# Performance work log

Measured on AMD Instinct MI355X. Metric: run time of the kernel, lower is better.

## Reference

```python
import jax, jax.numpy as jnp
import numpy as np

N_NODES = 25000
N_EDGES = 400000
N_GRAPHS = 64
F_IN = 128


def setup_inputs() -> dict:
    key = jax.random.key(0)
    ks = jax.random.split(key, 16)
    inp = {}
    inp["x"] = jax.random.normal(ks[0], (N_NODES, F_IN), dtype=jnp.float32)
    inp["edge_index"] = jax.random.randint(ks[1], (2, N_EDGES), 0, N_NODES, dtype=jnp.int64)
    inp["edge_attr"] = jax.random.uniform(ks[2], (N_EDGES,), dtype=jnp.float32)
    inp["batch_ids"] = jnp.sort(jax.random.randint(ks[3], (N_NODES,), 0, N_GRAPHS, dtype=jnp.int64))
    def lin(k, fan_in, fan_out):
        bound = 1.0 / np.sqrt(fan_in)
        return jax.random.uniform(k, (fan_in, fan_out), dtype=jnp.float32, minval=-bound, maxval=bound)
    inp["W1_rel"] = lin(ks[4], F_IN, 512)
    inp["b1"] = jnp.zeros((512,), jnp.float32)
    inp["W1_root"] = lin(ks[5], F_IN, 512)
    inp["W2_rel"] = lin(ks[6], 512, 512)
    inp["b2"] = jnp.zeros((512,), jnp.float32)
    inp["W2_root"] = lin(ks[7], 512, 512)
    inp["Wl1"] = lin(ks[8], 512, 64)
    inp["bl1"] = jnp.zeros((64,), jnp.float32)
    inp["Wl2"] = lin(ks[9], 64, 16)
    inp["bl2"] = jnp.zeros((16,), jnp.float32)
    inp["Wl3"] = lin(ks[10], 16, 1)
    inp["bl3"] = jnp.zeros((1,), jnp.float32)
    return inp


def _graph_conv(h, src, dst, edge_attr, W_rel, b_rel, W_root, n_nodes):
    # PyG GraphConv: lin_rel(scatter_add(w_e * x_src, dst)) + lin_root(x)
    msg = h[src] * edge_attr[:, None]                       # [E, F] gather
    agg = jax.ops.segment_sum(msg, dst, num_segments=n_nodes)  # [N, F] scatter-add
    return agg @ W_rel + b_rel + h @ W_root


def reference(x, edge_index, edge_attr, batch_ids, W1_rel, b1, W1_root,
              W2_rel, b2, W2_root, Wl1, bl1, Wl2, bl2, Wl3, bl3):
    n_nodes = x.shape[0]
    src, dst = edge_index[0], edge_index[1]
    h = jax.nn.relu(_graph_conv(x, src, dst, edge_attr, W1_rel, b1, W1_root, n_nodes))
    h = jax.nn.relu(_graph_conv(h, src, dst, edge_attr, W2_rel, b2, W2_root, n_nodes))
    # global mean pool by graph id
    sums = jax.ops.segment_sum(h, batch_ids, num_segments=N_GRAPHS)  # [G, 512]
    counts = jax.ops.segment_sum(jnp.ones((n_nodes,), h.dtype), batch_ids, num_segments=N_GRAPHS)
    g = sums / jnp.maximum(counts, 1.0)[:, None]
    # dropout is identity in eval mode
    g = jax.nn.relu(g @ Wl1 + bl1)
    g = jax.nn.relu(g @ Wl2 + bl2)
    return g @ Wl3 + bl3  # [G, 1]
```

## Files before the change

### kernel.cpp

```cpp
#include <hip/hip_runtime.h>
#include <hip/hip_bf16.h>
#include <hip/hip_fp16.h>
#include <stdint.h>

#define N_NODESC 25000
#define N_EDGESC 400000
#define N_GRAPHSC 64
#define F_INC 128
#define HIDC 512
#define PSTRIDE 1600000

typedef __attribute__((ext_vector_type(8))) short short8;
typedef __attribute__((ext_vector_type(8))) _Float16 half8;
typedef __attribute__((ext_vector_type(4))) float f32x4;

__device__ __forceinline__ unsigned short f2h(float f) {
  return __half_as_ushort(__float2half_rn(f));
}

__global__ __launch_bounds__(256)
void prep_kernel(const float* __restrict__ x, const int* __restrict__ ei,
                 const float* __restrict__ W1rel, const float* __restrict__ W1root,
                 const float* __restrict__ W2rel, const float* __restrict__ W2root,
                 unsigned short* __restrict__ xp, unsigned short* __restrict__ W1T,
                 unsigned short* __restrict__ W2T, int* __restrict__ deg,
                 float* __restrict__ gsum) {
  int blk = blockIdx.x, t = threadIdx.x;
  if (blk < 1563) {
    int e = blk * 256 + t;
    if (e < N_EDGESC) atomicAdd(&deg[ei[N_EDGESC + e]], 1);
  } else if (blk < 4688) {
    int idx = ((blk - 1563) * 256 + t) * 4;
    int node = idx >> 7;
    int col = idx & 127;
    float4 v = *(const float4*)(x + idx);
    ushort4 o;
    o.x = f2h(v.x); o.y = f2h(v.y); o.z = f2h(v.z); o.w = f2h(v.w);
    *(ushort4*)(xp + (size_t)(col >> 6) * PSTRIDE + (size_t)node * 64 + (col & 63)) = o;
  } else if (blk < 4848) {
    __shared__ float tile[64][65];
    int b2 = blk - 4688;
    const float* src;
    unsigned short* dst;
    int n0, k0, Kout;
    if (b2 < 128) {
      int kt = b2 >> 3, nt = b2 & 7;
      k0 = kt * 64; n0 = nt * 64;
      src = (k0 < 512) ? (W2rel + (size_t)k0 * 512) : (W2root + (size_t)(k0 - 512) * 512);
      dst = W2T; Kout = 1024;
    } else {
      int b = b2 - 128;
      int kt = b >> 3, nt = b & 7;
      k0 = kt * 64; n0 = nt * 64;
      src = (k0 < 128) ? (W1rel + (size_t)k0 * 512) : (W1root + (size_t)(k0 - 128) * 512);
      dst = W1T; Kout = 256;
    }
    int c = t & 63;
    int r4 = t >> 6;
#pragma unroll
    for (int rr = 0; rr < 64; rr += 4) {
      int row = rr + r4;
      tile[c][row] = src[(size_t)row * 512 + n0 + c];
    }
    __syncthreads();
#pragma unroll
    for (int rr = 0; rr < 64; rr += 4) {
      int nrow = rr + r4;
      dst[(size_t)(n0 + nrow) * Kout + k0 + c] = f2h(tile[nrow][c]);
    }
  } else {
    int i = (blk - 4848) * 256 + t;
    if (i < N_GRAPHSC * HIDC) gsum[i] = 0.f;
  }
}

__global__ __launch_bounds__(1024)
void scan_kernel(const int* __restrict__ deg, int* __restrict__ indptr, int* __restrict__ cursor,
                 int* __restrict__ sorted) {
  __shared__ int binsS[1024];
  __shared__ int scan2[1024];
  __shared__ int Wsh[16];
  __shared__ int waveBase[16];
  __shared__ int gTot;
  const int t = threadIdx.x;
  const int w = t >> 6;
  const int lane = t & 63;
  const int stripe = t & 3;
  const int nbase = w * 1600;
  const unsigned ub = (unsigned)deg[N_NODESC];
  binsS[t] = 0;
  __syncthreads();

  int dl[25];
  int tw = 0;
#pragma unroll
  for (int i = 0; i < 25; ++i) {
    int idx = nbase + i * 64 + lane;
    int d = (idx < N_NODESC) ? (int)((unsigned)deg[idx] - ub) : 0;
    dl[i] = d;
    if (idx < N_NODESC) {
      tw += d;
      atomicAdd(&binsS[(d > 255 ? 255 : d) * 4 + stripe], 1);
    }
  }
#pragma unroll
  for (int off = 32; off > 0; off >>= 1) tw += __shfl_xor(tw, off);
  if (lane == 0) Wsh[w] = tw;
  __syncthreads();

  if (t < 16) {
    int v = Wsh[t];
    int s = v;
#pragma unroll
    for (int off = 1; off < 16; off <<= 1) {
      int u = __shfl_up(s, off);
      if (t >= off) s += u;
    }
    waveBase[t] = s - v;
    if (t == 15) gTot = s;
  }
  int bv = binsS[t];
  scan2[t] = bv;
  __syncthreads();
  for (int off = 1; off < 1024; off <<= 1) {
    int v2 = (t >= off) ? scan2[t - off] : 0;
    __syncthreads();
    scan2[t] += v2;
    __syncthreads();
  }
  binsS[t] = scan2[t] - bv;
  __syncthreads();

  int run = waveBase[w];
#pragma unroll
  for (int i = 0; i < 25; ++i) {
    int idx = nbase + i * 64 + lane;
    int d = dl[i];
    int s = d;
#pragma unroll
    for (int off = 1; off < 64; off <<= 1) {
      int u = __shfl_up(s, off);
      if (lane >= off) s += u;
    }
    int excl = run + s - d;
    if (idx < N_NODESC) {
      indptr[idx] = excl;
      cursor[idx] = excl;
      int fb = (d > 255 ? 255 : d) * 4 + stripe;
      int pos = atomicAdd(&binsS[fb], 1);
      sorted[pos] = idx;
    }
    run += __shfl(s, 63);
  }
  if (t == 0) indptr[N_NODESC] = gTot;
}

__global__ void fill_kernel(const int* __restrict__ ei, const float* __restrict__ ea,
                            int* __restrict__ cursor, unsigned* __restrict__ emeta) {
  int e = blockIdx.x * blockDim.x + threadIdx.x;
  if (e >= N_EDGESC) return;
  int dst = ei[N_EDGESC + e];
  int pos = atomicAdd(&cursor[dst], 1);
  unsigned short hw = __half_as_ushort(__float2half_rn(ea[e]));
  emeta[pos] = (unsigned)ei[e] | ((unsigned)hw << 16);
}

__global__ __launch_bounds__(256)
void agg_gather_s(const unsigned short* __restrict__ feat, const int* __restrict__ indptr,
                  const unsigned* __restrict__ emeta, const int* __restrict__ sorted,
                  unsigned short* __restrict__ outp, int lgP) {
  int panel = blockIdx.x & ((1 << lgP) - 1);
  int nidx = (blockIdx.x >> lgP) * 32 + (threadIdx.x >> 3);
  if (nidx >= N_NODESC) return;
  int c8 = threadIdx.x & 7;
  int node = sorted[nidx];
  int beg = indptr[node];
  int deg = indptr[node + 1] - beg;
  const unsigned* mp = emeta + beg;
  const char* fb = (const char*)(feat + (size_t)panel * PSTRIDE);
  unsigned coff = c8 * 16u;
  float acc0[8] = {}, acc1[8] = {};
  int j = 0;
  for (; j + 4 <= deg; j += 4) {
    unsigned m0_ = mp[j];
    unsigned m1_ = mp[j + 1];
    unsigned m2_ = mp[j + 2];
    unsigned m3_ = mp[j + 3];
    half8 v0 = *(const half8*)(fb + (m0_ & 0xffffu) * 128u + coff);
    half8 v1 = *(const half8*)(fb + (m1_ & 0xffffu) * 128u + coff);
    half8 v2 = *(const half8*)(fb + (m2_ & 0xffffu) * 128u + coff);
    half8 v3 = *(const half8*)(fb + (m3_ & 0xffffu) * 128u + coff);
    float w0 = __half2float(__ushort_as_half((unsigned short)(m0_ >> 16)));
    float w1 = __half2float(__ushort_as_half((unsigned short)(m1_ >> 16)));
    float w2 = __half2float(__ushort_as_half((unsigned short)(m2_ >> 16)));
    float w3 = __half2float(__ushort_as_half((unsigned short)(m3_ >> 16)));
#pragma unroll
    for (int c = 0; c < 8; ++c) acc0[c] += (float)v0[c] * w0;
#pragma unroll
    for (int c = 0; c < 8; ++c) acc1[c] += (float)v1[c] * w1;
#pragma unroll
    for (int c = 0; c < 8; ++c) acc0[c] += (float)v2[c] * w2;
#pragma unroll
    for (int c = 0; c < 8; ++c) acc1[c] += (float)v3[c] * w3;
  }
  if (j + 2 <= deg) {
    unsigned mA = mp[j];
    unsigned mB = mp[j + 1];
    half8 vA = *(const half8*)(fb + (mA & 0xffffu) * 128u + coff);
    half8 vB = *(const half8*)(fb + (mB & 0xffffu) * 128u + coff);
    float wA = __half2float(__ushort_as_half((unsigned short)(mA >> 16)));
    float wB = __half2float(__ushort_as_half((unsigned short)(mB >> 16)));
#pragma unroll
    for (int c = 0; c < 8; ++c) acc0[c] += (float)vA[c] * wA;
#pragma unroll
    for (int c = 0; c < 8; ++c) acc1[c] += (float)vB[c] * wB;
    j += 2;
  }
  if (j < deg) {
    unsigned mA = mp[j];
    half8 vA = *(const half8*)(fb + (mA & 0xffffu) * 128u + coff);
    float wA = __half2float(__ushort_as_half((unsigned short)(mA >> 16)));
#pragma unroll
    for (int c = 0; c < 8; ++c) acc0[c] += (float)vA[c] * wA;
  }
  half8 o;
#pragma unroll
  for (int c = 0; c < 8; ++c) o[c] = (_Float16)(acc0[c] + acc1[c]);
  *(half8*)(outp + (size_t)panel * PSTRIDE + (size_t)node * 64 + c8 * 8) = o;
}

__device__ __forceinline__ void gemm_map3(int b, int& m0, int& n0) {
  int g = (b & 7) * 98 + (b >> 3);
  m0 = (g >> 2) << 7;
  n0 = (g & 3) << 7;
}

__device__ __forceinline__ void stage_a(const short* Apan, int m0, int M,
                                        short* dst, int wave, int lane) {
#pragma unroll
  for (int i = 0; i < 4; ++i) {
    int s = ((i * 4 + wave) << 6) + lane;
    int row = s >> 3;
    int c = (s & 7) ^ (row & 7);
    int rg = m0 + row;
    if (rg > M - 1) rg = M - 1;
    const short* gp = Apan + (size_t)rg * 64 + (c << 3);
    __builtin_amdgcn_global_load_lds(
        (const __attribute__((address_space(1))) void*)gp,
        (__attribute__((address_space(3))) void*)(dst + ((i * 4 + wave) << 9)),
        16, 0, 0);
  }
}

__device__ __forceinline__ void stage_b(const short* BT, int n0, int K, int kbase,
                                        short* dst, int wave, int lane) {
#pragma unroll
  for (int i = 0; i < 4; ++i) {
    int s = ((i * 4 + wave) << 6) + lane;
    int row = s >> 3;
    int c = (s & 7) ^ (row & 7);
    const short* gp = BT + (size_t)(n0 + row) * K + kbase + (c << 3);
    __builtin_amdgcn_global_load_lds(
        (const __attribute__((address_space(1))) void*)gp,
        (__attribute__((address_space(3))) void*)(dst + ((i * 4 + wave) << 9)),
        16, 0, 0);
  }
}

__device__ __forceinline__ const short* apan_sel(const short* A0, const short* A1,
                                                 int S, int kt) {
  int kb = kt << 6;
  const short* Ab = (kb < S) ? A0 : A1;
  int koff = (kb < S) ? kb : kb - S;
  return Ab + (size_t)(koff >> 6) * PSTRIDE;
}

__device__ __forceinline__ void wg_barrier() {
  asm volatile("" ::: "memory");
  __builtin_amdgcn_s_barrier();
  asm volatile("" ::: "memory");
}

__device__ __forceinline__ void gemm_core(const short* A0, const short* A1,
                                          const short* BT, int M, int S,
                                          int m0, int n0, short* As, short* Bs,
                                          f32x4 (&acc)[4][4]) {
  const int K = 2 * S;
  const int nk = K >> 6;
  const int tid = threadIdx.x;
  const int wave = tid >> 6;
  const int lane = tid & 63;
  const int quad = lane >> 4;
  const int r = lane & 15;
  const int wm = (wave >> 1) << 6;
  const int wn = (wave & 1) << 6;

  int aoff[2][4], boff[2][4];
#pragma unroll
  for (int p = 0; p < 2; ++p) {
#pragma unroll
    for (int tm = 0; tm < 4; ++tm) {
      int ml = wm + tm * 16 + r;
      int c = (p << 2) + quad;
      aoff[p][tm] = (ml * 8 + (c ^ (ml & 7))) * 8;
    }
#pragma unroll
    for (int tn = 0; tn < 4; ++tn) {
      int nl = wn + tn * 16 + r;
      int c = (p << 2) + quad;
      boff[p][tn] = (nl * 8 + (c ^ (nl & 7))) * 8;
    }
  }

  stage_a(apan_sel(A0, A1, S, 0), m0, M, As, wave, lane);
  stage_b(BT, n0, K, 0, Bs, wave, lane);
  asm volatile("s_waitcnt vmcnt(0)");
  wg_barrier();

  for (int t = 0; t < nk; ++t) {
    const int cur = t & 1;
    const int nxt = cur ^ 1;
    int kt1 = (t + 1 < nk) ? t + 1 : nk - 1;
    stage_a(apan_sel(A0, A1, S, kt1), m0, M, As + nxt * 8192, wave, lane);
    stage_b(BT, n0, K, kt1 << 6, Bs + nxt * 8192, wave, lane);

    const short* Ac = As + cur * 8192;
    const short* Bc = Bs + cur * 8192;
    {
      half8 af[4], bf[4];
#pragma unroll
      for (int tm = 0; tm < 4; ++tm) af[tm] = *(const half8*)&Ac[aoff[0][tm]];
#pragma unroll
      for (int tn = 0; tn < 4; ++tn) bf[tn] = *(const half8*)&Bc[boff[0][tn]];
      __builtin_amdgcn_s_setprio(1);
#pragma unroll
      for (int tm = 0; tm < 4; ++tm)
#pragma unroll
        for (int tn = 0; tn < 4; ++tn)
          acc[tm][tn] = __builtin_amdgcn_mfma_f32_16x16x32_f16(af[tm], bf[tn], acc[tm][tn], 0, 0, 0);
      __builtin_amdgcn_s_setprio(0);
    }
    {
      half8 af[4], bf[4];
#pragma unroll
      for (int tm = 0; tm < 4; ++tm) af[tm] = *(const half8*)&Ac[aoff[1][tm]];
#pragma unroll
      for (int tn = 0; tn < 4; ++tn) bf[tn] = *(const half8*)&Bc[boff[1][tn]];
      __builtin_amdgcn_s_setprio(1);
#pragma unroll
      for (int tm = 0; tm < 4; ++tm)
#pragma unroll
        for (int tn = 0; tn < 4; ++tn)
          acc[tm][tn] = __builtin_amdgcn_mfma_f32_16x16x32_f16(af[tm], bf[tn], acc[tm][tn], 0, 0, 0);
      __builtin_amdgcn_s_setprio(0);
    }
    asm volatile("s_waitcnt vmcnt(0)");
    wg_barrier();
  }
}

__global__ __launch_bounds__(256, 2)
void gemm_bt_relu(const short* __restrict__ A0, const short* __restrict__ A1,
                  const short* __restrict__ BT, const float* __restrict__ bias,
                  unsigned short* __restrict__ Outp, int M, int S) {
  __shared__ __align__(16) short As[2 * 8192];
  __shared__ __align__(16) short Bs[2 * 8192];
  int m0, n0;
  gemm_map3(blockIdx.x, m0, n0);
  const int wave = threadIdx.x >> 6;
  const int lane = threadIdx.x & 63;
  const int quad = lane >> 4;
  const int r = lane & 15;
  const int wm = (wave >> 1) << 6;
  const int wn = (wave & 1) << 6;

  f32x4 acc[4][4] = {};
  gemm_core(A0, A1, BT, M, S, m0, n0, As, Bs, acc);

#pragma unroll
  for (int tm = 0; tm < 4; ++tm) {
    int rowb = m0 + wm + tm * 16 + quad * 4;
#pragma unroll
    for (int tn = 0; tn < 4; ++tn) {
      int col = n0 + wn + tn * 16 + r;
      float bv = bias[col];
      unsigned short* obase = Outp + (size_t)(col >> 6) * PSTRIDE + (col & 63);
#pragma unroll
      for (int reg = 0; reg < 4; ++reg) {
        int rr = rowb + reg;
        if (rr < M) {
          float v = acc[tm][tn][reg] + bv;
          v = v > 0.f ? v : 0.f;
          obase[(size_t)rr * 64] = f2h(v);
        }
      }
    }
  }
}

__global__ __launch_bounds__(256, 2)
void gemm_bt_pool(const short* __restrict__ A0, const short* __restrict__ A1,
                  const short* __restrict__ BT, const float* __restrict__ bias,
                  const int* __restrict__ batch, float* __restrict__ gsum, int M, int S) {
  __shared__ __align__(16) short As[2 * 8192];
  __shared__ __align__(16) short Bs[2 * 8192];
  int m0, n0;
  gemm_map3(blockIdx.x, m0, n0);
  const int wave = threadIdx.x >> 6;
  const int lane = threadIdx.x & 63;
  const int quad = lane >> 4;
  const int r = lane & 15;
  const int wm = (wave >> 1) << 6;
  const int wn = (wave & 1) << 6;

  f32x4 acc[4][4] = {};
  gemm_core(A0, A1, BT, M, S, m0, n0, As, Bs, acc);

  int gid[4][4];
#pragma unroll
  for (int tm = 0; tm < 4; ++tm) {
    int rowb = m0 + wm + tm * 16 + quad * 4;
#pragma unroll
    for (int reg = 0; reg < 4; ++reg) {
      int rr = rowb + reg;
      gid[tm][reg] = batch[rr < M ? rr : (M - 1)];
    }
#pragma unroll
    for (int tn = 0; tn < 4; ++tn) {
      float bv = bias[n0 + wn + tn * 16 + r];
#pragma unroll
      for (int reg = 0; reg < 4; ++reg) {
        int rr = rowb + reg;
        float v = acc[tm][tn][reg] + bv;
        v = v > 0.f ? v : 0.f;
        acc[tm][tn][reg] = (rr < M) ? v : 0.f;
      }
    }
  }
  int g_lo = batch[m0 < M ? m0 : (M - 1)];
  int g_hi = batch[(m0 + 127) < M ? (m0 + 127) : (M - 1)];
  for (int g = g_lo; g <= g_hi; ++g) {
#pragma unroll
    for (int tn = 0; tn < 4; ++tn) {
      float s = 0.f;
#pragma unroll
      for (int tm = 0; tm < 4; ++tm)
#pragma unroll
        for (int reg = 0; reg < 4; ++reg)
          s += (gid[tm][reg] == g) ? acc[tm][tn][reg] : 0.f;
      s += __shfl_xor(s, 16);
      s += __shfl_xor(s, 32);
      if (quad == 0)
        atomicAdd(&gsum[(size_t)g * HIDC + n0 + wn + tn * 16 + r], s);
    }
  }
}

__global__ __launch_bounds__(256)
void mlp_kernel(const float* __restrict__ gsum, const int* __restrict__ batch,
                const float* __restrict__ Wl1, const float* __restrict__ bl1,
                const float* __restrict__ Wl2, const float* __restrict__ bl2,
                const float* __restrict__ Wl3, const float* __restrict__ bl3,
                float* __restrict__ out) {
  int gi = blockIdx.x;
  int t = threadIdx.x;
  int unit = t & 63;
  int part = t >> 6;
  __shared__ float red[4][64];
  __shared__ float h1s[64];
  __shared__ float h2s[16];
  int lo = 0, hi = N_NODESC;
  while (lo < hi) { int mid = (lo + hi) >> 1; if (batch[mid] < gi) lo = mid + 1; else hi = mid; }
  int start = lo;
  hi = N_NODESC;
  while (lo < hi) { int mid = (lo + hi) >> 1; if (batch[mid] < gi + 1) lo = mid + 1; else hi = mid; }
  float inv = 1.0f / fmaxf((float)(lo - start), 1.0f);
  const float* gr = gsum + gi * HIDC;
  float acc = 0.f;
  for (int j = part * 128; j < (part + 1) * 128; ++j)
    acc += gr[j] * Wl1[j * 64 + unit];
  red[part][unit] = acc;
  __syncthreads();
  if (t < 64) {
    float a = bl1[t] + (red[0][t] + red[1][t] + red[2][t] + red[3][t]) * inv;
    h1s[t] = fmaxf(a, 0.f);
  }
  __syncthreads();
  if (t < 16) {
    float a = bl2[t];
    for (int j = 0; j < 64; ++j) a += h1s[j] * Wl2[j * 16 + t];
    h2s[t] = fmaxf(a, 0.f);
  }
  __syncthreads();
  if (t == 0) {
    float a = bl3[0];
    for (int j = 0; j < 16; ++j) a += h2s[j] * Wl3[j];
    out[gi] = a;
  }
}

extern "C" void kernel_launch(void* const* d_in, const int* in_sizes, int n_in,
                              void* d_out, int out_size, void* d_ws, size_t ws_size,
                              hipStream_t stream) {
  const float* x      = (const float*)d_in[0];
  const int*   ei     = (const int*)d_in[1];
  const float* ea     = (const float*)d_in[2];
  const int*   batch  = (const int*)d_in[3];
  const float* W1rel  = (const float*)d_in[4];
  const float* b1     = (const float*)d_in[5];
  const float* W1root = (const float*)d_in[6];
  const float* W2rel  = (const float*)d_in[7];
  const float* b2     = (const float*)d_in[8];
  const float* W2root = (const float*)d_in[9];
  const float* Wl1    = (const float*)d_in[10];
  const float* bl1    = (const float*)d_in[11];
  const float* Wl2    = (const float*)d_in[12];
  const float* bl2    = (const float*)d_in[13];
  const float* Wl3    = (const float*)d_in[14];
  const float* bl3    = (const float*)d_in[15];
  float* out = (float*)d_out;

  char* ws = (char*)d_ws;
  unsigned short* xp     = (unsigned short*)(ws + 0);
  unsigned short* agg1p  = (unsigned short*)(ws + 6400000);
  unsigned short* h1p    = (unsigned short*)(ws + 12800000);
  unsigned short* agg2p  = (unsigned short*)(ws + 38400000);
  unsigned short* W1T    = (unsigned short*)(ws + 64000000);
  unsigned short* W2T    = (unsigned short*)(ws + 64262144);
  float*          gsum   = (float*)(ws + 65310720);
  int*            deg    = (int*)(ws + 65441792);
  int*            cursor = (int*)(ws + 65541796);
  int*            indptr = (int*)(ws + 65641796);
  unsigned*       emeta  = (unsigned*)(ws + 65741812);
  int*            sorted = (int*)(ws + 67341812);

  prep_kernel<<<4976, 256, 0, stream>>>(x, ei, W1rel, W1root, W2rel, W2root,
                                        xp, W1T, W2T, deg, gsum);
  scan_kernel<<<1, 1024, 0, stream>>>(deg, indptr, cursor, sorted);
  fill_kernel<<<(N_EDGESC + 255) / 256, 256, 0, stream>>>(ei, ea, cursor, emeta);

  const int NBLK = (N_NODESC + 31) / 32;
  agg_gather_s<<<NBLK * 2, 256, 0, stream>>>(xp, indptr, emeta, sorted, agg1p, 1);

  gemm_bt_relu<<<784, 256, 0, stream>>>((const short*)agg1p, (const short*)xp,
                                        (const short*)W1T, b1, h1p, N_NODESC, 128);

  agg_gather_s<<<NBLK * 8, 256, 0, stream>>>(h1p, indptr, emeta, sorted, agg2p, 3);

  gemm_bt_pool<<<784, 256, 0, stream>>>((const short*)agg2p, (const short*)h1p,
                                        (const short*)W2T, b2, batch, gsum, N_NODESC, 512);

  mlp_kernel<<<N_GRAPHSC, 256, 0, stream>>>(gsum, batch, Wl1, bl1, Wl2, bl2, Wl3, bl3, out);
}
```

Baseline: 285.3 us.

## Enlarge GEMM tile to 256x128 and drop LDS double buffering

Both GEMM kernels move from 128x128 to 256x128 tiles, with each wave computing 128x64 using 8x4 MFMA accumulators, and the grid halves from 784 to 392 blocks. The double-buffered prefetch is replaced by a single-buffer loop: load, wait, barrier, compute, barrier. The aim is more reuse of each B tile and fewer blocks, at the cost of exposed global-load latency each k-step. Register pressure also rises, which may spill under launch_bounds(256,2), and 392 blocks may underfill the 256 CUs.

```diff
diff --git a/kernel.cpp b/kernel.cpp
--- a/kernel.cpp
+++ b/kernel.cpp
@@ -229,16 +229,16 @@
   *(half8*)(outp + (size_t)panel * PSTRIDE + (size_t)node * 64 + c8 * 8) = o;
 }
 
-__device__ __forceinline__ void gemm_map3(int b, int& m0, int& n0) {
-  int g = (b & 7) * 98 + (b >> 3);
-  m0 = (g >> 2) << 7;
+__device__ __forceinline__ void gemm_map4(int b, int& m0, int& n0) {
+  int g = (b & 7) * 49 + (b >> 3);
+  m0 = (g >> 2) << 8;
   n0 = (g & 3) << 7;
 }
 
-__device__ __forceinline__ void stage_a(const short* Apan, int m0, int M,
-                                        short* dst, int wave, int lane) {
-#pragma unroll
-  for (int i = 0; i < 4; ++i) {
+__device__ __forceinline__ void stage_a8(const short* Apan, int m0, int M,
+                                         short* dst, int wave, int lane) {
+#pragma unroll
+  for (int i = 0; i < 8; ++i) {
     int s = ((i * 4 + wave) << 6) + lane;
     int row = s >> 3;
     int c = (s & 7) ^ (row & 7);
@@ -252,8 +252,8 @@
   }
 }
 
-__device__ __forceinline__ void stage_b(const short* BT, int n0, int K, int kbase,
-                                        short* dst, int wave, int lane) {
+__device__ __forceinline__ void stage_b4(const short* BT, int n0, int K, int kbase,
+                                         short* dst, int wave, int lane) {
 #pragma unroll
   for (int i = 0; i < 4; ++i) {
     int s = ((i * 4 + wave) << 6) + lane;
@@ -284,7 +284,7 @@
 __device__ __forceinline__ void gemm_core(const short* A0, const short* A1,
                                           const short* BT, int M, int S,
                                           int m0, int n0, short* As, short* Bs,
-                                          f32x4 (&acc)[4][4]) {
+                                          f32x4 (&acc)[8][4]) {
   const int K = 2 * S;
   const int nk = K >> 6;
   const int tid = threadIdx.x;
@@ -292,14 +292,14 @@
   const int lane = tid & 63;
   const int quad = lane >> 4;
   const int r = lane & 15;
-  const int wm = (wave >> 1) << 6;
+  const int wm = (wave >> 1) << 7;
   const int wn = (wave & 1) << 6;
 
-  int aoff[2][4], boff[2][4];
+  int aoff[2][8], boff[2][4];
 #pragma unroll
   for (int p = 0; p < 2; ++p) {
 #pragma unroll
-    for (int tm = 0; tm < 4; ++tm) {
+    for (int tm = 0; tm < 8; ++tm) {
       int ml = wm + tm * 16 + r;
       int c = (p << 2) + quad;
       aoff[p][tm] = (ml * 8 + (c ^ (ml & 7))) * 8;
@@ -312,49 +312,39 @@
     }
   }
 
-  stage_a(apan_sel(A0, A1, S, 0), m0, M, As, wave, lane);
-  stage_b(BT, n0, K, 0, Bs, wave, lane);
-  asm volatile("s_waitcnt vmcnt(0)");
-  wg_barrier();
-
   for (int t = 0; t < nk; ++t) {
-    const int cur = t & 1;
-    const int nxt = cur ^ 1;
-    int kt1 = (t + 1 < nk) ? t + 1 : nk - 1;
-    stage_a(apan_sel(A0, A1, S, kt1), m0, M, As + nxt * 8192, wave, lane);
-    stage_b(BT, n0, K, kt1 << 6, Bs + nxt * 8192, wave, lane);
-
-    const short* Ac = As + cur * 8192;
-    const short* Bc = Bs + cur * 8192;
+    stage_a8(apan_sel(A0, A1, S, t), m0, M, As, wave, lane);
+    stage_b4(BT, n0, K, t << 6, Bs, wave, lane);
+    asm volatile("s_waitcnt vmcnt(0)");
+    wg_barrier();
     {
-      half8 af[4], bf[4];
-#pragma unroll
-      for (int tm = 0; tm < 4; ++tm) af[tm] = *(const half8*)&Ac[aoff[0][tm]];
-#pragma unroll
-      for (int tn = 0; tn < 4; ++tn) bf[tn] = *(const half8*)&Bc[boff[0][tn]];
+      half8 af[8], bf[4];
+#pragma unroll
+      for (int tm = 0; tm < 8; ++tm) af[tm] = *(const half8*)&As[aoff[0][tm]];
+#pragma unroll
+      for (int tn = 0; tn < 4; ++tn) bf[tn] = *(const half8*)&Bs[boff[0][tn]];
       __builtin_amdgcn_s_setprio(1);
 #pragma unroll
-      for (int tm = 0; tm < 4; ++tm)
+      for (int tm = 0; tm < 8; ++tm)
 #pragma unroll
         for (int tn = 0; tn < 4; ++tn)
           acc[tm][tn] = __builtin_amdgcn_mfma_f32_16x16x32_f16(af[tm], bf[tn], acc[tm][tn], 0, 0, 0);
       __builtin_amdgcn_s_setprio(0);
     }
     {
-      half8 af[4], bf[4];
-#pragma unroll
-      for (int tm = 0; tm < 4; ++tm) af[tm] = *(const half8*)&Ac[aoff[1][tm]];
-#pragma unroll
-      for (int tn = 0; tn < 4; ++tn) bf[tn] = *(const half8*)&Bc[boff[1][tn]];
+      half8 af[8], bf[4];
+#pragma unroll
+      for (int tm = 0; tm < 8; ++tm) af[tm] = *(const half8*)&As[aoff[1][tm]];
+#pragma unroll
+      for (int tn = 0; tn < 4; ++tn) bf[tn] = *(const half8*)&Bs[boff[1][tn]];
       __builtin_amdgcn_s_setprio(1);
 #pragma unroll
-      for (int tm = 0; tm < 4; ++tm)
+      for (int tm = 0; tm < 8; ++tm)
 #pragma unroll
         for (int tn = 0; tn < 4; ++tn)
           acc[tm][tn] = __builtin_amdgcn_mfma_f32_16x16x32_f16(af[tm], bf[tn], acc[tm][tn], 0, 0, 0);
       __builtin_amdgcn_s_setprio(0);
     }
-    asm volatile("s_waitcnt vmcnt(0)");
     wg_barrier();
   }
 }
@@ -363,22 +353,22 @@
 void gemm_bt_relu(const short* __restrict__ A0, const short* __restrict__ A1,
                   const short* __restrict__ BT, const float* __restrict__ bias,
                   unsigned short* __restrict__ Outp, int M, int S) {
-  __shared__ __align__(16) short As[2 * 8192];
-  __shared__ __align__(16) short Bs[2 * 8192];
+  __shared__ __align__(16) short As[256 * 64];
+  __shared__ __align__(16) short Bs[128 * 64];
   int m0, n0;
-  gemm_map3(blockIdx.x, m0, n0);
+  gemm_map4(blockIdx.x, m0, n0);
   const int wave = threadIdx.x >> 6;
   const int lane = threadIdx.x & 63;
   const int quad = lane >> 4;
   const int r = lane & 15;
-  const int wm = (wave >> 1) << 6;
+  const int wm = (wave >> 1) << 7;
   const int wn = (wave & 1) << 6;
 
-  f32x4 acc[4][4] = {};
+  f32x4 acc[8][4] = {};
   gemm_core(A0, A1, BT, M, S, m0, n0, As, Bs, acc);
 
 #pragma unroll
-  for (int tm = 0; tm < 4; ++tm) {
+  for (int tm = 0; tm < 8; ++tm) {
     int rowb = m0 + wm + tm * 16 + quad * 4;
 #pragma unroll
     for (int tn = 0; tn < 4; ++tn) {
@@ -402,23 +392,23 @@
 void gemm_bt_pool(const short* __restrict__ A0, const short* __restrict__ A1,
                   const short* __restrict__ BT, const float* __restrict__ bias,
                   const int* __restrict__ batch, float* __restrict__ gsum, int M, int S) {
-  __shared__ __align__(16) short As[2 * 8192];
-  __shared__ __align__(16) short Bs[2 * 8192];
+  __shared__ __align__(16) short As[256 * 64];
+  __shared__ __align__(16) short Bs[128 * 64];
   int m0, n0;
-  gemm_map3(blockIdx.x, m0, n0);
+  gemm_map4(blockIdx.x, m0, n0);
   const int wave = threadIdx.x >> 6;
   const int lane = threadIdx.x & 63;
   const int quad = lane >> 4;
   const int r = lane & 15;
-  const int wm = (wave >> 1) << 6;
+  const int wm = (wave >> 1) << 7;
   const int wn = (wave & 1) << 6;
 
-  f32x4 acc[4][4] = {};
+  f32x4 acc[8][4] = {};
   gemm_core(A0, A1, BT, M, S, m0, n0, As, Bs, acc);
 
-  int gid[4][4];
-#pragma unroll
-  for (int tm = 0; tm < 4; ++tm) {
+  int gid[8][4];
+#pragma unroll
+  for (int tm = 0; tm < 8; ++tm) {
     int rowb = m0 + wm + tm * 16 + quad * 4;
 #pragma unroll
     for (int reg = 0; reg < 4; ++reg) {
@@ -438,13 +428,13 @@
     }
   }
   int g_lo = batch[m0 < M ? m0 : (M - 1)];
-  int g_hi = batch[(m0 + 127) < M ? (m0 + 127) : (M - 1)];
+  int g_hi = batch[(m0 + 255) < M ? (m0 + 255) : (M - 1)];
   for (int g = g_lo; g <= g_hi; ++g) {
 #pragma unroll
     for (int tn = 0; tn < 4; ++tn) {
       float s = 0.f;
 #pragma unroll
-      for (int tm = 0; tm < 4; ++tm)
+      for (int tm = 0; tm < 8; ++tm)
 #pragma unroll
         for (int reg = 0; reg < 4; ++reg)
           s += (gid[tm][reg] == g) ? acc[tm][tn][reg] : 0.f;
@@ -542,12 +532,12 @@
   const int NBLK = (N_NODESC + 31) / 32;
   agg_gather_s<<<NBLK * 2, 256, 0, stream>>>(xp, indptr, emeta, sorted, agg1p, 1);
 
-  gemm_bt_relu<<<784, 256, 0, stream>>>((const short*)agg1p, (const short*)xp,
+  gemm_bt_relu<<<392, 256, 0, stream>>>((const short*)agg1p, (const short*)xp,
                                         (const short*)W1T, b1, h1p, N_NODESC, 128);
 
   agg_gather_s<<<NBLK * 8, 256, 0, stream>>>(h1p, indptr, emeta, sorted, agg2p, 3);
 
-  gemm_bt_pool<<<784, 256, 0, stream>>>((const short*)agg2p, (const short*)h1p,
+  gemm_bt_pool<<<392, 256, 0, stream>>>((const short*)agg2p, (const short*)h1p,
                                         (const short*)W2T, b2, batch, gsum, N_NODESC, 512);
 
   mlp_kernel<<<N_GRAPHSC, 256, 0, stream>>>(gsum, batch, Wl1, bl1, Wl2, bl2, Wl3, bl3, out);
```

Result: faster. 270.3 us (median of 2 runs) (-5.3%).
